# Optimization experiments

Hardware: AMD Instinct MI355X
Metric: run time of the kernel (lower is better)

The kernel has to match this reference:

```python
import jax, jax.numpy as jnp
import numpy as np

DIM = 512
N_LAYERS = 2
N_HEADS = 8
HEAD_DIM = DIM // N_HEADS
VOCAB = 50257
MAX_SEQ = 2048
N_LEVELS = 3  # len(chunk_sizes)
HID = 4 * DIM
B, S = 2, 1024
STD = 0.02
EPS = 1e-5


def setup_inputs() -> dict:
    key = jax.random.key(0)
    ks = jax.random.split(key, 12)
    f32 = jnp.float32
    inp = {}
    inp["input_ids"] = jax.random.randint(ks[0], (B, S), 0, VOCAB)
    inp["tok_emb"] = jax.random.normal(ks[1], (VOCAB, DIM), f32) * STD  # tied with head
    inp["pos_emb"] = jax.random.normal(ks[2], (MAX_SEQ, DIM), f32) * STD
    # attention projections, stored [in, out] so y = x @ W (math-equivalent to torch x @ W.T)
    inp["Wq"] = jax.random.normal(ks[3], (N_LAYERS, DIM, DIM), f32) * STD
    inp["Wk"] = jax.random.normal(ks[4], (N_LAYERS, DIM, DIM), f32) * STD
    inp["Wv"] = jax.random.normal(ks[5], (N_LAYERS, DIM, DIM), f32) * STD
    inp["Wo"] = jax.random.normal(ks[6], (N_LAYERS, DIM, DIM), f32) * STD
    # layer norms
    inp["ln1_g"] = jnp.ones((N_LAYERS, DIM), f32)
    inp["ln1_b"] = jnp.zeros((N_LAYERS, DIM), f32)
    inp["ln2_g"] = jnp.ones((N_LAYERS, DIM), f32)
    inp["ln2_b"] = jnp.zeros((N_LAYERS, DIM), f32)
    inp["lnf_g"] = jnp.ones((DIM,), f32)
    inp["lnf_b"] = jnp.zeros((DIM,), f32)
    # continuum memory system: N_LEVELS chained MLPs per layer
    inp["W1"] = jax.random.normal(ks[7], (N_LAYERS, N_LEVELS, DIM, HID), f32) * STD
    inp["b1"] = jnp.zeros((N_LAYERS, N_LEVELS, HID), f32)
    inp["W2"] = jax.random.normal(ks[8], (N_LAYERS, N_LEVELS, HID, DIM), f32) * STD
    inp["b2"] = jnp.zeros((N_LAYERS, N_LEVELS, DIM), f32)
    return inp


def layer_norm(x, g, b):
    mu = jnp.mean(x, axis=-1, keepdims=True)
    var = jnp.var(x, axis=-1, keepdims=True)
    return (x - mu) / jnp.sqrt(var + EPS) * g + b


def linear_attention_with_memory(x, Wq, Wk, Wv, Wo):
    # x: [B, S, D]. Fast-weight recurrence: M_t = M_{t-1} + v_t k_t^T ; y_t = M_t q_t
    Bsz, Slen, D = x.shape
    H, hd = N_HEADS, HEAD_DIM

    def proj(W):  # -> [S, B, H, hd] (time-major for scan)
        return jnp.moveaxis((x @ W).reshape(Bsz, Slen, H, hd), 1, 0)

    q, k, v = proj(Wq), proj(Wk), proj(Wv)
    M0 = jnp.zeros((Bsz, H, hd, hd), x.dtype)

    def step(M, qkv):
        q_t, k_t, v_t = qkv
        M = M + jnp.einsum('bhd,bhk->bhdk', v_t, k_t)
        y_t = jnp.einsum('bhdk,bhk->bhd', M, q_t)
        return M, y_t

    _, ys = jax.lax.scan(step, M0, (q, k, v))  # ys: [S, B, H, hd]
    y = jnp.moveaxis(ys, 0, 1).reshape(Bsz, Slen, D)
    return y @ Wo


def cms(x, W1, b1, W2, b2):
    # chained MLP levels (dropout=0 / eval mode)
    for m in range(W1.shape[0]):
        x = jax.nn.gelu(x @ W1[m] + b1[m]) @ W2[m] + b2[m]
    return x


def reference(input_ids, tok_emb, pos_emb, Wq, Wk, Wv, Wo,
              ln1_g, ln1_b, ln2_g, ln2_b, lnf_g, lnf_b,
              W1, b1, W2, b2):
    Bsz, Slen = input_ids.shape
    x = tok_emb[input_ids] + pos_emb[:Slen][None, :, :]
    for l in range(Wq.shape[0]):
        x = x + linear_attention_with_memory(layer_norm(x, ln1_g[l], ln1_b[l]),
                                             Wq[l], Wk[l], Wv[l], Wo[l])
        x = x + cms(layer_norm(x, ln2_g[l], ln2_b[l]), W1[l], b1[l], W2[l], b2[l])
    x = layer_norm(x, lnf_g, lnf_b)
    logits = x @ tok_emb.T  # tied head
    return logits
```

## Files before the change

kernel.cpp:

```cpp
#include <hip/hip_runtime.h>
#include <hip/hip_bf16.h>
#include <cstdint>

using bf16 = __hip_bfloat16;
typedef __attribute__((ext_vector_type(8))) __bf16 bf16x8;
typedef __attribute__((ext_vector_type(4))) float f32x4;
typedef __attribute__((ext_vector_type(4))) unsigned int u32x4;

#define SEQ    1024
#define BATCH  2
#define ROWS   (BATCH*SEQ)
#define DMODEL 512
#define HIDDEN 2048
#define NHEADS 8
#define HD     64
#define VOCABN 50257
#define CHUNK  32
#define NCHUNK (SEQ/CHUNK)
#define QKVW   1536

__device__ __forceinline__ float gelu_tanh(float x) {
  float u = 0.7978845608028654f * (x + 0.044715f * x * x * x);
  return 0.5f * x * (1.0f + tanhf(u));
}

__global__ __launch_bounds__(512, 2)
void head_gemm8(const bf16* __restrict__ A, const bf16* __restrict__ Bt,
                float* __restrict__ C, int N, int ntn)
{
  constexpr int NT = 8;
  extern __shared__ char smem[];
  bf16* Al = (bf16*)smem;
  bf16* Bl = (bf16*)(smem + 65536);
  const int t = threadIdx.x, lane = t & 63;
  const int w = t >> 6, wm = w >> 2, wn = w & 3;
  const int tm = blockIdx.x & 7, tn = blockIdx.x >> 3;
  const int arow0 = tm * 256, brow0 = tn * 256;
  const int ko0 = lane >> 4;
  const int kph1 = ((ko0 ^ (lane & 7)) << 4);
  const int kph2 = kph1 ^ 64;

  f32x4 acc[2][2][4][2];
#pragma unroll
  for (int i = 0; i < 2; ++i)
#pragma unroll
    for (int j = 0; j < 2; ++j)
#pragma unroll
      for (int m = 0; m < 4; ++m)
#pragma unroll
        for (int n = 0; n < 2; ++n) acc[i][j][m][n] = (f32x4){0.f, 0.f, 0.f, 0.f};

  auto stageA = [&](int s, int half, bf16* dstbuf) {
#pragma unroll
    for (int rep = 0; rep < 2; ++rep) {
      int slot = rep * 512 + t;
      int row = slot >> 3, ko = slot & 7;
      int kosrc = ko ^ (row & 7);
      const bf16* src = A + (size_t)(arow0 + half * 128 + row) * 512 + s * 64 + kosrc * 8;
      bf16* dst = dstbuf + (half * 128 + row) * 64 + ko * 8;
      __builtin_amdgcn_global_load_lds(
          (const __attribute__((address_space(1))) unsigned int*)src,
          (__attribute__((address_space(3))) unsigned int*)dst, 16, 0, 0);
    }
  };
  auto stageB = [&](int s, int half, bf16* dstbuf) {
#pragma unroll
    for (int rep = 0; rep < 2; ++rep) {
      int slot = rep * 512 + t;
      int row = slot >> 3, ko = slot & 7;
      int kosrc = ko ^ (row & 7);
      int br = brow0 + half * 128 + row; br = br < N ? br : N - 1;
      const bf16* src = Bt + (size_t)br * 512 + s * 64 + kosrc * 8;
      bf16* dst = dstbuf + (half * 128 + row) * 64 + ko * 8;
      __builtin_amdgcn_global_load_lds(
          (const __attribute__((address_space(1))) unsigned int*)src,
          (__attribute__((address_space(3))) unsigned int*)dst, 16, 0, 0);
    }
  };

  bf16* Ac = Al;
  bf16* Bc = Bl;
  bf16* An = Al + 16384;
  bf16* Bn = Bl + 16384;

  stageA(0, 0, Ac); stageB(0, 0, Bc); stageA(0, 1, Ac); stageB(0, 1, Bc);
  stageA(1, 0, An); stageB(1, 0, Bn);
  asm volatile("s_waitcnt vmcnt(4)" ::: "memory");
  asm volatile("s_barrier" ::: "memory");

#define PH(MH, NH, AC, BC, STAGE_STMT, WAIT_STMT) do {                          \
    bf16x8 a_[4][2], b_[2][2];                                                  \
    _Pragma("unroll") for (int fm = 0; fm < 4; ++fm) {                          \
      const char* ap = (const char*)(AC) +                                      \
          ((MH) * 128 + wm * 64 + fm * 16 + (lane & 15)) * 128;                 \
      a_[fm][0] = __builtin_bit_cast(bf16x8, *(const u32x4*)(ap + kph1));       \
      a_[fm][1] = __builtin_bit_cast(bf16x8, *(const u32x4*)(ap + kph2));       \
    }                                                                           \
    _Pragma("unroll") for (int fn = 0; fn < 2; ++fn) {                          \
      const char* bp = (const char*)(BC) +                                      \
          ((NH) * 128 + wn * 32 + fn * 16 + (lane & 15)) * 128;                 \
      b_[fn][0] = __builtin_bit_cast(bf16x8, *(const u32x4*)(bp + kph1));       \
      b_[fn][1] = __builtin_bit_cast(bf16x8, *(const u32x4*)(bp + kph2));       \
    }                                                                           \
    STAGE_STMT;                                                                 \
    asm volatile("s_barrier" ::: "memory");                                     \
    asm volatile("s_waitcnt lgkmcnt(0)" ::: "memory");                          \
    __builtin_amdgcn_sched_barrier(0);                                          \
    __builtin_amdgcn_s_setprio(1);                                              \
    _Pragma("unroll") for (int fm = 0; fm < 4; ++fm)                            \
      _Pragma("unroll") for (int fn = 0; fn < 2; ++fn) {                        \
        acc[MH][NH][fm][fn] = __builtin_amdgcn_mfma_f32_16x16x32_bf16(          \
            a_[fm][0], b_[fn][0], acc[MH][NH][fm][fn], 0, 0, 0);                \
        acc[MH][NH][fm][fn] = __builtin_amdgcn_mfma_f32_16x16x32_bf16(          \
            a_[fm][1], b_[fn][1], acc[MH][NH][fm][fn], 0, 0, 0);                \
      }                                                                         \
    __builtin_amdgcn_s_setprio(0);                                              \
    WAIT_STMT;                                                                  \
    asm volatile("s_barrier" ::: "memory");                                     \
  } while (0)

#pragma unroll
  for (int I = 0; I < NT / 2; ++I) {
    const int u = 2 * I;
    PH(0, 0, Ac, Bc, { stageA(u + 1, 1, An); }, {});
    PH(0, 1, Ac, Bc, { stageB(u + 1, 1, Bn); }, {});
    PH(1, 0, Ac, Bc, { if (u + 2 < NT) stageA(u + 2, 0, Ac); }, {});
    PH(1, 1, Ac, Bc, { if (u + 2 < NT) stageB(u + 2, 0, Bc); },
       { if (u + 2 < NT) asm volatile("s_waitcnt vmcnt(4)" ::: "memory");
         else            asm volatile("s_waitcnt vmcnt(0)" ::: "memory"); });
    PH(0, 0, An, Bn, { if (u + 2 < NT) stageA(u + 2, 1, Ac); }, {});
    PH(0, 1, An, Bn, { if (u + 2 < NT) stageB(u + 2, 1, Bc); }, {});
    PH(1, 0, An, Bn, { if (u + 3 < NT) stageA(u + 3, 0, An); }, {});
    PH(1, 1, An, Bn, { if (u + 3 < NT) stageB(u + 3, 0, Bn); },
       { if (u + 2 < NT) {
           if (u + 3 < NT) asm volatile("s_waitcnt vmcnt(4)" ::: "memory");
           else            asm volatile("s_waitcnt vmcnt(0)" ::: "memory");
         } });
  }
#undef PH

#pragma unroll
  for (int mh = 0; mh < 2; ++mh)
#pragma unroll
    for (int fm = 0; fm < 4; ++fm) {
      int row = arow0 + mh * 128 + wm * 64 + fm * 16 + (lane >> 4) * 4;
#pragma unroll
      for (int nh = 0; nh < 2; ++nh)
#pragma unroll
        for (int fn = 0; fn < 2; ++fn) {
          int col = brow0 + nh * 128 + wn * 32 + fn * 16 + (lane & 15);
          if (col < N) {
#pragma unroll
            for (int r = 0; r < 4; ++r)
              C[(size_t)(row + r) * N + col] = acc[mh][nh][fm][fn][r];
          }
        }
    }
}

template<int EPI>
__global__ __launch_bounds__(256, 4)
void gemm_mid(const bf16* __restrict__ A, const bf16* __restrict__ Bt,
              void* __restrict__ Cout, const float* __restrict__ bias,
              int M, int N, int K, int Ks, int ldc, int ntn)
{
  __shared__ __align__(16) bf16 As[128 * 64];
  __shared__ __align__(16) bf16 Bs[64 * 64];
  const int t = threadIdx.x;
  const int lane = t & 63;
  const int w = t >> 6;
  const int wr = w >> 1, wc = w & 1;
  const int tm = blockIdx.x / ntn, tn = blockIdx.x % ntn;
  const int sk = blockIdx.y;
  const int kbeg = sk * Ks;
  const int rA = lane & 15;
  const int ko0 = lane >> 4;

  f32x4 acc[4][2];
#pragma unroll
  for (int m = 0; m < 4; ++m)
#pragma unroll
    for (int n = 0; n < 2; ++n) acc[m][n] = (f32x4){0.f, 0.f, 0.f, 0.f};

  for (int k0 = kbeg; k0 < kbeg + Ks; k0 += 64) {
#pragma unroll
    for (int rep = 0; rep < 4; ++rep) {
      int c = rep * 256 + t;
      int row = c >> 3, ko = c & 7;
      const bf16* ga = A + (size_t)(tm * 128 + row) * K + k0 + (ko ^ (row & 7)) * 8;
      __builtin_amdgcn_global_load_lds(
          (const __attribute__((address_space(1))) unsigned int*)ga,
          (__attribute__((address_space(3))) unsigned int*)(As + row * 64 + ko * 8),
          16, 0, 0);
    }
#pragma unroll
    for (int rep = 0; rep < 2; ++rep) {
      int c = rep * 256 + t;
      int row = c >> 3, ko = c & 7;
      const bf16* gb = Bt + (size_t)(tn * 64 + row) * K + k0 + (ko ^ (row & 7)) * 8;
      __builtin_amdgcn_global_load_lds(
          (const __attribute__((address_space(1))) unsigned int*)gb,
          (__attribute__((address_space(3))) unsigned int*)(Bs + row * 64 + ko * 8),
          16, 0, 0);
    }
    asm volatile("s_waitcnt vmcnt(0)" ::: "memory");
    __syncthreads();

    {
      bf16x8 af[4], bfv[2];
#pragma unroll
      for (int m = 0; m < 4; ++m) {
        int row = wr * 64 + m * 16 + rA;
        af[m] = __builtin_bit_cast(bf16x8,
            *(const u32x4*)((const char*)As + row * 128 + ((ko0 ^ (row & 7)) << 4)));
      }
#pragma unroll
      for (int n = 0; n < 2; ++n) {
        int row = wc * 32 + n * 16 + rA;
        bfv[n] = __builtin_bit_cast(bf16x8,
            *(const u32x4*)((const char*)Bs + row * 128 + ((ko0 ^ (row & 7)) << 4)));
      }
#pragma unroll
      for (int m = 0; m < 4; ++m)
#pragma unroll
        for (int n = 0; n < 2; ++n)
          acc[m][n] = __builtin_amdgcn_mfma_f32_16x16x32_bf16(af[m], bfv[n], acc[m][n], 0, 0, 0);
    }
    {
      bf16x8 af[4], bfv[2];
#pragma unroll
      for (int m = 0; m < 4; ++m) {
        int row = wr * 64 + m * 16 + rA;
        af[m] = __builtin_bit_cast(bf16x8,
            *(const u32x4*)((const char*)As + row * 128 + (((ko0 ^ (row & 7)) << 4) ^ 64)));
      }
#pragma unroll
      for (int n = 0; n < 2; ++n) {
        int row = wc * 32 + n * 16 + rA;
        bfv[n] = __builtin_bit_cast(bf16x8,
            *(const u32x4*)((const char*)Bs + row * 128 + (((ko0 ^ (row & 7)) << 4) ^ 64)));
      }
#pragma unroll
      for (int m = 0; m < 4; ++m)
#pragma unroll
        for (int n = 0; n < 2; ++n)
          acc[m][n] = __builtin_amdgcn_mfma_f32_16x16x32_bf16(af[m], bfv[n], acc[m][n], 0, 0, 0);
    }
    __syncthreads();
  }

#pragma unroll
  for (int m = 0; m < 4; ++m) {
    const int row = tm * 128 + wr * 64 + m * 16 + (lane >> 4) * 4;
#pragma unroll
    for (int n = 0; n < 2; ++n) {
      const int col = tn * 64 + wc * 32 + n * 16 + rA;
#pragma unroll
      for (int r = 0; r < 4; ++r) {
        float v = acc[m][n][r];
        if (EPI == 0) {
          ((float*)Cout)[(size_t)(row + r) * ldc + col] = v;
        } else if (EPI == 1) {
          ((float*)Cout)[(size_t)sk * M * N + (size_t)(row + r) * N + col] = v;
        } else {
          v += bias[col]; v = gelu_tanh(v);
          ((bf16*)Cout)[(size_t)(row + r) * ldc + col] = __float2bfloat16(v);
        }
      }
    }
  }
}

__global__ __launch_bounds__(256, 2)
void gemm_bt(const bf16* __restrict__ A, const bf16* __restrict__ Bt,
             void* __restrict__ Cout, const float* __restrict__ bias,
             int M, int N, int K, int ldc, int ntn)
{
  __shared__ __align__(16) bf16 As[128 * 32];
  __shared__ __align__(16) bf16 Bs[128 * 32];
  const int t = threadIdx.x;
  const int lane = t & 63;
  const int w = t >> 6;
  const int wr = w >> 1, wc = w & 1;
  const int tile = blockIdx.x;
  const int tm = tile / ntn, tn = tile % ntn;

  f32x4 acc[4][4];
#pragma unroll
  for (int m = 0; m < 4; ++m)
#pragma unroll
    for (int n = 0; n < 4; ++n) acc[m][n] = (f32x4){0.f, 0.f, 0.f, 0.f};

  const int rA = lane & 15;
  const int kq = (lane >> 4) * 8;
  const size_t a_row0 = (size_t)tm * 128;
  const int b_row0 = tn * 128;

  for (int k0 = 0; k0 < K; k0 += 32) {
#pragma unroll
    for (int i = 0; i < 2; ++i) {
      int chunk = i * 256 + t;
      int row = chunk >> 2;
      int kc = (chunk & 3) * 8;
      const bf16* ga = A + (a_row0 + row) * K + k0 + kc;
      int brow = b_row0 + row; brow = brow < N ? brow : N - 1;
      const bf16* gb = Bt + (size_t)brow * K + k0 + kc;
      __builtin_amdgcn_global_load_lds(
          (const __attribute__((address_space(1))) unsigned int*)ga,
          (__attribute__((address_space(3))) unsigned int*)(As + (size_t)(i * 256 + w * 64) * 8),
          16, 0, 0);
      __builtin_amdgcn_global_load_lds(
          (const __attribute__((address_space(1))) unsigned int*)gb,
          (__attribute__((address_space(3))) unsigned int*)(Bs + (size_t)(i * 256 + w * 64) * 8),
          16, 0, 0);
    }
    asm volatile("s_waitcnt vmcnt(0)" ::: "memory");
    __syncthreads();

    bf16x8 af[4], bfv[4];
#pragma unroll
    for (int m = 0; m < 4; ++m)
      af[m] = __builtin_bit_cast(bf16x8, *(const u32x4*)(As + (wr * 64 + m * 16 + rA) * 32 + kq));
#pragma unroll
    for (int n = 0; n < 4; ++n)
      bfv[n] = __builtin_bit_cast(bf16x8, *(const u32x4*)(Bs + (wc * 64 + n * 16 + rA) * 32 + kq));
#pragma unroll
    for (int m = 0; m < 4; ++m)
#pragma unroll
      for (int n = 0; n < 4; ++n)
        acc[m][n] = __builtin_amdgcn_mfma_f32_16x16x32_bf16(af[m], bfv[n], acc[m][n], 0, 0, 0);
    __syncthreads();
  }

#pragma unroll
  for (int m = 0; m < 4; ++m) {
    const int row = tm * 128 + wr * 64 + m * 16 + (lane >> 4) * 4;
#pragma unroll
    for (int n = 0; n < 4; ++n) {
      const int col = tn * 128 + wc * 64 + n * 16 + (lane & 15);
      if (col < N) {
#pragma unroll
        for (int r = 0; r < 4; ++r)
          ((float*)Cout)[(size_t)(row + r) * ldc + col] = acc[m][n][r];
      }
    }
  }
}

__global__ __launch_bounds__(256)
void reduce_bias_bf16(const float* __restrict__ part, bf16* __restrict__ out,
                      const float* __restrict__ bias)
{
  int i = blockIdx.x * 256 + threadIdx.x;
  const float4* p4 = (const float4*)part;
  const size_t str = (size_t)ROWS * DMODEL / 4;
  float4 v = p4[i];
  float4 v1 = p4[i + str], v2 = p4[i + 2 * str], v3 = p4[i + 3 * str];
  v.x += v1.x + v2.x + v3.x; v.y += v1.y + v2.y + v3.y;
  v.z += v1.z + v2.z + v3.z; v.w += v1.w + v2.w + v3.w;
  float4 bb = ((const float4*)bias)[i & (DMODEL / 4 - 1)];
  v.x += bb.x; v.y += bb.y; v.z += bb.z; v.w += bb.w;
  union { bf16 h[4]; uint2 u; } cv;
  cv.h[0] = __float2bfloat16(v.x); cv.h[1] = __float2bfloat16(v.y);
  cv.h[2] = __float2bfloat16(v.z); cv.h[3] = __float2bfloat16(v.w);
  ((uint2*)out)[i] = cv.u;
}

template<bool BIAS>
__global__ __launch_bounds__(256)
void reduce_resid_ln(const float* __restrict__ part, float* __restrict__ x,
                     const float* __restrict__ bias, const float* __restrict__ g,
                     const float* __restrict__ b, bf16* __restrict__ xn)
{
  int lane = threadIdx.x & 63;
  int row = blockIdx.x * 4 + (threadIdx.x >> 6);
  const float4* p4 = (const float4*)part;
  const size_t str = (size_t)ROWS * DMODEL / 4;
  size_t base = (size_t)row * (DMODEL / 4) + lane * 2;
  float4 a0 = p4[base], a1 = p4[base + 1];
#pragma unroll
  for (int s = 1; s < 4; ++s) {
    float4 q0 = p4[base + s * str], q1 = p4[base + 1 + s * str];
    a0.x += q0.x; a0.y += q0.y; a0.z += q0.z; a0.w += q0.w;
    a1.x += q1.x; a1.y += q1.y; a1.z += q1.z; a1.w += q1.w;
  }
  if (BIAS) {
    float4 b0 = ((const float4*)bias)[lane * 2];
    float4 b1 = ((const float4*)bias)[lane * 2 + 1];
    a0.x += b0.x; a0.y += b0.y; a0.z += b0.z; a0.w += b0.w;
    a1.x += b1.x; a1.y += b1.y; a1.z += b1.z; a1.w += b1.w;
  }
  float4* xr = (float4*)(x + (size_t)row * DMODEL);
  float4 x0 = xr[lane * 2], x1 = xr[lane * 2 + 1];
  x0.x += a0.x; x0.y += a0.y; x0.z += a0.z; x0.w += a0.w;
  x1.x += a1.x; x1.y += a1.y; x1.z += a1.z; x1.w += a1.w;
  xr[lane * 2] = x0; xr[lane * 2 + 1] = x1;
  float s  = x0.x + x0.y + x0.z + x0.w + x1.x + x1.y + x1.z + x1.w;
  float ss = x0.x*x0.x + x0.y*x0.y + x0.z*x0.z + x0.w*x0.w
           + x1.x*x1.x + x1.y*x1.y + x1.z*x1.z + x1.w*x1.w;
#pragma unroll
  for (int off = 32; off > 0; off >>= 1) { s += __shfl_xor(s, off); ss += __shfl_xor(ss, off); }
  float mu = s * (1.f / DMODEL);
  float inv = rsqrtf(ss * (1.f / DMODEL) - mu * mu + 1e-5f);
  int c0 = lane * 8;
  float vv[8] = {x0.x, x0.y, x0.z, x0.w, x1.x, x1.y, x1.z, x1.w};
#pragma unroll
  for (int j = 0; j < 8; ++j)
    xn[(size_t)row * DMODEL + c0 + j] = __float2bfloat16((vv[j] - mu) * inv * g[c0 + j] + b[c0 + j]);
}

__global__ __launch_bounds__(256)
void embed_ln(const int* __restrict__ ids, const float* __restrict__ te,
              const float* __restrict__ pe, const float* __restrict__ g,
              const float* __restrict__ b, float* __restrict__ x, bf16* __restrict__ xn)
{
  int lane = threadIdx.x & 63;
  int row = blockIdx.x * 4 + (threadIdx.x >> 6);
  int sq = row & (SEQ - 1);
  int id = ids[row];
  const float4* tr = (const float4*)(te + (size_t)id * DMODEL);
  const float4* pr = (const float4*)(pe + (size_t)sq * DMODEL);
  float4 x0 = tr[lane * 2], x1 = tr[lane * 2 + 1];
  float4 p0 = pr[lane * 2], p1 = pr[lane * 2 + 1];
  x0.x += p0.x; x0.y += p0.y; x0.z += p0.z; x0.w += p0.w;
  x1.x += p1.x; x1.y += p1.y; x1.z += p1.z; x1.w += p1.w;
  float4* xr = (float4*)(x + (size_t)row * DMODEL);
  xr[lane * 2] = x0; xr[lane * 2 + 1] = x1;
  float s  = x0.x + x0.y + x0.z + x0.w + x1.x + x1.y + x1.z + x1.w;
  float ss = x0.x*x0.x + x0.y*x0.y + x0.z*x0.z + x0.w*x0.w
           + x1.x*x1.x + x1.y*x1.y + x1.z*x1.z + x1.w*x1.w;
#pragma unroll
  for (int off = 32; off > 0; off >>= 1) { s += __shfl_xor(s, off); ss += __shfl_xor(ss, off); }
  float mu = s * (1.f / DMODEL);
  float inv = rsqrtf(ss * (1.f / DMODEL) - mu * mu + 1e-5f);
  int c0 = lane * 8;
  float vv[8] = {x0.x, x0.y, x0.z, x0.w, x1.x, x1.y, x1.z, x1.w};
#pragma unroll
  for (int j = 0; j < 8; ++j)
    xn[(size_t)row * DMODEL + c0 + j] = __float2bfloat16((vv[j] - mu) * inv * g[c0 + j] + b[c0 + j]);
}

__global__ __launch_bounds__(256)
void transpose_cvt(const float* __restrict__ in, bf16* __restrict__ out, int R, int C)
{
  __shared__ float tile[32][33];
  int mat = blockIdx.z;
  const float* src = in + (size_t)mat * R * C;
  bf16* dst = out + (size_t)mat * R * C;
  int c0 = blockIdx.x * 32, r0 = blockIdx.y * 32;
  int tx = threadIdx.x, ty = threadIdx.y;
#pragma unroll
  for (int i = ty; i < 32; i += 8)
    tile[i][tx] = src[(size_t)(r0 + i) * C + c0 + tx];
  __syncthreads();
#pragma unroll
  for (int i = ty; i < 32; i += 8)
    dst[(size_t)(c0 + i) * R + r0 + tx] = __float2bfloat16(tile[tx][i]);
}

__global__ __launch_bounds__(256)
void transpose_qkv(const float* __restrict__ Wq, const float* __restrict__ Wk,
                   const float* __restrict__ Wv, bf16* __restrict__ out)
{
  __shared__ float tile[32][33];
  int z = blockIdx.z;
  int l = z / 3, p = z % 3;
  const float* src = (p == 0 ? Wq : (p == 1 ? Wk : Wv)) + (size_t)l * DMODEL * DMODEL;
  bf16* dst = out + (size_t)l * QKVW * DMODEL + (size_t)p * DMODEL * DMODEL;
  int c0 = blockIdx.x * 32, r0 = blockIdx.y * 32;
  int tx = threadIdx.x, ty = threadIdx.y;
#pragma unroll
  for (int i = ty; i < 32; i += 8)
    tile[i][tx] = src[(size_t)(r0 + i) * DMODEL + c0 + tx];
  __syncthreads();
#pragma unroll
  for (int i = ty; i < 32; i += 8)
    dst[(size_t)(c0 + i) * DMODEL + r0 + tx] = __float2bfloat16(tile[tx][i]);
}

__global__ void cvt_bf16_k(const float* __restrict__ in, bf16* __restrict__ out, int n4)
{
  int i = blockIdx.x * 256 + threadIdx.x;
  if (i >= n4) return;
  float4 v = ((const float4*)in)[i];
  union { bf16 h[4]; uint2 u; } cv;
  cv.h[0] = __float2bfloat16(v.x); cv.h[1] = __float2bfloat16(v.y);
  cv.h[2] = __float2bfloat16(v.z); cv.h[3] = __float2bfloat16(v.w);
  ((uint2*)out)[i] = cv.u;
}

__global__ __launch_bounds__(256)
void scan_ktv(const float* __restrict__ qkv, float* __restrict__ ktv)
{
  int blk = blockIdx.x;
  int c = blk & (NCHUNK - 1), bh = blk >> 5;
  int b = bh >> 3, h = bh & 7;
  __shared__ float ks[CHUNK][64], vs[CHUNK][64];
  int t = threadIdx.x;
  size_t base = ((size_t)(b * SEQ + c * CHUNK)) * QKVW + h * HD;
#pragma unroll
  for (int i = 0; i < CHUNK * 64 / 256; ++i) {
    int idx = i * 256 + t;
    int s = idx >> 6, e = idx & 63;
    ks[s][e] = qkv[base + 512 + (size_t)s * QKVW + e];
    vs[s][e] = qkv[base + 1024 + (size_t)s * QKVW + e];
  }
  __syncthreads();
  int e = t >> 2, d0 = (t & 3) * 16;
  float acc[16];
#pragma unroll
  for (int j = 0; j < 16; ++j) acc[j] = 0.f;
  for (int s = 0; s < CHUNK; ++s) {
    float kv = ks[s][e];
#pragma unroll
    for (int j = 0; j < 16; ++j) acc[j] += kv * vs[s][d0 + j];
  }
  float* o = ktv + (size_t)blk * 4096 + e * 64 + d0;
#pragma unroll
  for (int j = 0; j < 16; ++j) o[j] = acc[j];
}

__global__ __launch_bounds__(256)
void scan_attn(const float* __restrict__ qkv, const float* __restrict__ ktv,
               bf16* __restrict__ y)
{
  int blk = blockIdx.x;
  int c = blk & (NCHUNK - 1), bh = blk >> 5;
  int b = bh >> 3, h = bh & 7;
  __shared__ float qs[CHUNK][65], ks[CHUNK][65], vs[CHUNK][65];
  __shared__ float Ss[CHUNK][CHUNK + 1];
  __shared__ float Ms[64][65];
  int t = threadIdx.x;
  size_t base = ((size_t)(b * SEQ + c * CHUNK)) * QKVW + h * HD;
#pragma unroll
  for (int i = 0; i < CHUNK * 64 / 256; ++i) {
    int idx = i * 256 + t;
    int s = idx >> 6, e = idx & 63;
    qs[s][e] = qkv[base + (size_t)s * QKVW + e];
    ks[s][e] = qkv[base + 512 + (size_t)s * QKVW + e];
    vs[s][e] = qkv[base + 1024 + (size_t)s * QKVW + e];
  }
  {
    int e = t >> 2, d0 = (t & 3) * 16;
    float mp[16];
#pragma unroll
    for (int j = 0; j < 16; ++j) mp[j] = 0.f;
    for (int cp = 0; cp < c; ++cp) {
      const float* p = ktv + ((size_t)bh * NCHUNK + cp) * 4096 + e * 64 + d0;
#pragma unroll
      for (int j = 0; j < 16; ++j) mp[j] += p[j];
    }
#pragma unroll
    for (int j = 0; j < 16; ++j) Ms[e][d0 + j] = mp[j];
  }
  __syncthreads();
  {
    int si = t >> 3, j0 = (t & 7) * 4;
    float sa[4] = {0.f, 0.f, 0.f, 0.f};
    for (int e = 0; e < 64; ++e) {
      float qv = qs[si][e];
#pragma unroll
      for (int j = 0; j < 4; ++j) sa[j] += qv * ks[j0 + j][e];
    }
#pragma unroll
    for (int j = 0; j < 4; ++j) Ss[si][j0 + j] = (j0 + j <= si) ? sa[j] : 0.f;
  }
  __syncthreads();
  {
    int si = t >> 3, d0 = (t & 7) * 8;
    float ya[8];
#pragma unroll
    for (int j = 0; j < 8; ++j) ya[j] = 0.f;
    for (int sp = 0; sp < CHUNK; ++sp) {
      float sv = Ss[si][sp];
#pragma unroll
      for (int j = 0; j < 8; ++j) ya[j] += sv * vs[sp][d0 + j];
    }
    for (int e = 0; e < 64; ++e) {
      float qv = qs[si][e];
#pragma unroll
      for (int j = 0; j < 8; ++j) ya[j] += qv * Ms[e][d0 + j];
    }
    bf16* o = y + ((size_t)(b * SEQ + c * CHUNK + si)) * DMODEL + h * HD + d0;
#pragma unroll
    for (int j = 0; j < 8; ++j) o[j] = __float2bfloat16(ya[j]);
  }
}

extern "C" void kernel_launch(void* const* d_in, const int* in_sizes, int n_in,
                              void* d_out, int out_size, void* d_ws, size_t ws_size,
                              hipStream_t stream)
{
  const int*   ids  = (const int*)  d_in[0];
  const float* tok  = (const float*)d_in[1];
  const float* pos  = (const float*)d_in[2];
  const float* Wq   = (const float*)d_in[3];
  const float* Wk   = (const float*)d_in[4];
  const float* Wv   = (const float*)d_in[5];
  const float* Wo   = (const float*)d_in[6];
  const float* ln1g = (const float*)d_in[7];
  const float* ln1b = (const float*)d_in[8];
  const float* ln2g = (const float*)d_in[9];
  const float* ln2b = (const float*)d_in[10];
  const float* lnfg = (const float*)d_in[11];
  const float* lnfb = (const float*)d_in[12];
  const float* W1   = (const float*)d_in[13];
  const float* b1   = (const float*)d_in[14];
  const float* W2   = (const float*)d_in[15];
  const float* b2   = (const float*)d_in[16];
  float* out = (float*)d_out;

  char* ws = (char*)d_ws;
  size_t off = 0;
  auto alloc = [&](size_t bytes) { void* p = ws + off; off += (bytes + 255) & ~(size_t)255; return p; };
  bf16* QKVt = (bf16*)alloc((size_t)2 * QKVW * 512 * 2);
  bf16* Wot  = (bf16*)alloc((size_t)2 * 512 * 512 * 2);
  bf16* W1t  = (bf16*)alloc((size_t)6 * 512 * 2048 * 2);
  bf16* W2t  = (bf16*)alloc((size_t)6 * 2048 * 512 * 2);
  bf16* tokb = (bf16*)alloc((size_t)VOCABN * 512 * 2);
  float* x   = (float*)alloc((size_t)ROWS * 512 * 4);
  bf16*  xn  = (bf16*) alloc((size_t)ROWS * 512 * 2);
  bf16*  tbuf= (bf16*) alloc((size_t)ROWS * 512 * 2);
  bf16*  hbuf= (bf16*) alloc((size_t)ROWS * 2048 * 2);
  float* qkvf= (float*)alloc((size_t)ROWS * QKVW * 4);
  bf16*  yb  = (bf16*) alloc((size_t)ROWS * 512 * 2);
  float* ktv = (float*)alloc((size_t)16 * NCHUNK * 4096 * 4);
  float* part= (float*)alloc((size_t)4 * ROWS * 512 * 4);

  dim3 tb(32, 8);
  transpose_qkv<<<dim3(16, 16, 6), tb, 0, stream>>>(Wq, Wk, Wv, QKVt);
  transpose_cvt<<<dim3(16, 16, 2), tb, 0, stream>>>(Wo, Wot, 512, 512);
  transpose_cvt<<<dim3(64, 16, 6), tb, 0, stream>>>(W1, W1t, 512, 2048);
  transpose_cvt<<<dim3(16, 64, 6), tb, 0, stream>>>(W2, W2t, 2048, 512);
  int n4 = VOCABN * 512 / 4;
  cvt_bf16_k<<<(n4 + 255) / 256, 256, 0, stream>>>(tok, tokb, n4);

  embed_ln<<<ROWS / 4, 256, 0, stream>>>(ids, tok, pos, ln1g, ln1b, x, xn);

  for (int l = 0; l < 2; ++l) {
    gemm_mid<0><<<dim3(16 * (QKVW / 64)), 256, 0, stream>>>(
        xn, QKVt + (size_t)l * QKVW * 512, qkvf, nullptr, ROWS, QKVW, 512, 512, QKVW, QKVW / 64);
    scan_ktv<<<16 * NCHUNK, 256, 0, stream>>>(qkvf, ktv);
    scan_attn<<<16 * NCHUNK, 256, 0, stream>>>(qkvf, ktv, yb);
    gemm_mid<1><<<dim3(16 * 8, 4), 256, 0, stream>>>(
        yb, Wot + (size_t)l * 512 * 512, part, nullptr, ROWS, 512, 512, 128, 512, 8);
    reduce_resid_ln<false><<<ROWS / 4, 256, 0, stream>>>(
        part, x, nullptr, ln2g + l * 512, ln2b + l * 512, xn);

    const bf16* cur = xn;
    for (int m = 0; m < 3; ++m) {
      int lm = l * 3 + m;
      gemm_mid<2><<<dim3(16 * (2048 / 64)), 256, 0, stream>>>(
          cur, W1t + (size_t)lm * 2048 * 512, hbuf, b1 + (size_t)lm * 2048,
          ROWS, 2048, 512, 512, 2048, 2048 / 64);
      gemm_mid<1><<<dim3(16 * 8, 4), 256, 0, stream>>>(
          hbuf, W2t + (size_t)lm * 512 * 2048, part, nullptr, ROWS, 512, 2048, 512, 512, 8);
      if (m < 2) {
        reduce_bias_bf16<<<ROWS * 512 / 4 / 256, 256, 0, stream>>>(part, tbuf, b2 + (size_t)lm * 512);
        cur = tbuf;
      } else {
        const float* g = (l == 0) ? (ln1g + 512) : lnfg;
        const float* b = (l == 0) ? (ln1b + 512) : lnfb;
        reduce_resid_ln<true><<<ROWS / 4, 256, 0, stream>>>(part, x, b2 + (size_t)lm * 512, g, b, xn);
      }
    }
  }

  int ntn_h = (VOCABN + 255) / 256;
  (void)hipFuncSetAttribute((const void*)head_gemm8,
                            hipFuncAttributeMaxDynamicSharedMemorySize, 131072);
  head_gemm8<<<dim3(8 * ntn_h), 512, 131072, stream>>>(xn, tokb, out, VOCABN, ntn_h);
  if (hipGetLastError() != hipSuccess) {
    gemm_bt<<<dim3((ROWS / 128) * ((VOCABN + 127) / 128)), 256, 0, stream>>>(
        xn, tokb, out, nullptr, ROWS, VOCABN, 512, VOCABN, (VOCABN + 127) / 128);
  }
}
```

Measured before the change: 588.9 us.

## Precompute exclusive prefix of chunk KV states and remap GEMM workgroups across XCDs

Adds a prefix_ktv kernel that converts the per-chunk k^T v states into exclusive prefix sums in place. scan_attn then reads a single 64x64 state per chunk instead of summing up to 31 earlier chunks, which removes quadratic global reads. The head GEMM and gemm_mid also remap blockIdx so tiles are assigned round-robin across the 8 XCDs, aiming for better L2 locality. The prefix pass is serial over chunks with only 16 blocks and adds a launch. The remap assumes the grid size is divisible by 8.

```diff
diff --git a/kernel.cpp b/kernel.cpp
--- a/kernel.cpp
+++ b/kernel.cpp
@@ -34,7 +34,8 @@
   bf16* Bl = (bf16*)(smem + 65536);
   const int t = threadIdx.x, lane = t & 63;
   const int w = t >> 6, wm = w >> 2, wn = w & 3;
-  const int tm = blockIdx.x & 7, tn = blockIdx.x >> 3;
+  const int wid = (blockIdx.x % 8) * ntn + (blockIdx.x / 8);
+  const int tm = wid & 7, tn = wid >> 3;
   const int arow0 = tm * 256, brow0 = tn * 256;
   const int ko0 = lane >> 4;
   const int kph1 = ((ko0 ^ (lane & 7)) << 4);
@@ -170,7 +171,9 @@
   const int lane = t & 63;
   const int w = t >> 6;
   const int wr = w >> 1, wc = w & 1;
-  const int tm = blockIdx.x / ntn, tn = blockIdx.x % ntn;
+  const int nwg = gridDim.x;
+  const int wid = (blockIdx.x % 8) * (nwg >> 3) + (blockIdx.x >> 3);
+  const int tm = wid / ntn, tn = wid % ntn;
   const int sk = blockIdx.y;
   const int kbeg = sk * Ks;
   const int rA = lane & 15;
@@ -521,6 +524,27 @@
 }
 
 __global__ __launch_bounds__(256)
+void prefix_ktv(float* __restrict__ ktv)
+{
+  int bh = blockIdx.x;
+  int t = threadIdx.x;
+  int e = t >> 2, d0 = (t & 3) * 16;
+  float run[16];
+#pragma unroll
+  for (int j = 0; j < 16; ++j) run[j] = 0.f;
+  for (int cp = 0; cp < NCHUNK; ++cp) {
+    float* p = ktv + ((size_t)bh * NCHUNK + cp) * 4096 + e * 64 + d0;
+    float tmp[16];
+#pragma unroll
+    for (int j = 0; j < 16; ++j) tmp[j] = p[j];
+#pragma unroll
+    for (int j = 0; j < 16; ++j) p[j] = run[j];
+#pragma unroll
+    for (int j = 0; j < 16; ++j) run[j] += tmp[j];
+  }
+}
+
+__global__ __launch_bounds__(256)
 void scan_attn(const float* __restrict__ qkv, const float* __restrict__ ktv,
                bf16* __restrict__ y)
 {
@@ -542,16 +566,9 @@
   }
   {
     int e = t >> 2, d0 = (t & 3) * 16;
-    float mp[16];
-#pragma unroll
-    for (int j = 0; j < 16; ++j) mp[j] = 0.f;
-    for (int cp = 0; cp < c; ++cp) {
-      const float* p = ktv + ((size_t)bh * NCHUNK + cp) * 4096 + e * 64 + d0;
-#pragma unroll
-      for (int j = 0; j < 16; ++j) mp[j] += p[j];
-    }
-#pragma unroll
-    for (int j = 0; j < 16; ++j) Ms[e][d0 + j] = mp[j];
+    const float* p = ktv + ((size_t)bh * NCHUNK + c) * 4096 + e * 64 + d0;
+#pragma unroll
+    for (int j = 0; j < 16; ++j) Ms[e][d0 + j] = p[j];
   }
   __syncthreads();
   {
@@ -641,6 +658,7 @@
     gemm_mid<0><<<dim3(16 * (QKVW / 64)), 256, 0, stream>>>(
         xn, QKVt + (size_t)l * QKVW * 512, qkvf, nullptr, ROWS, QKVW, 512, 512, QKVW, QKVW / 64);
     scan_ktv<<<16 * NCHUNK, 256, 0, stream>>>(qkvf, ktv);
+    prefix_ktv<<<16, 256, 0, stream>>>(ktv);
     scan_attn<<<16 * NCHUNK, 256, 0, stream>>>(qkvf, ktv, yb);
     gemm_mid<1><<<dim3(16 * 8, 4), 256, 0, stream>>>(
         yb, Wot + (size_t)l * 512 * 512, part, nullptr, ROWS, 512, 512, 128, 512, 8);
```

Measured after the change: 604.9 us. 1.03x slower.
